# Kernel optimization log

Hardware: AMD Instinct MI355X
Metric: run time of the kernel (lower is better)

Reference implementation:

```python
import jax, jax.numpy as jnp
import numpy as np

B, S, D, E, N, K = 4, 2048, 1024, 2048, 16, 4

def setup_inputs() -> dict:
    key = jax.random.key(0)
    ks = jax.random.split(key, 16)
    w = lambda k, shape, s=0.02: jax.random.normal(k, shape, dtype=jnp.float32) * s
    return {
        "x": jax.random.normal(ks[0], (B, S, D), dtype=jnp.float32),
        "ln_g": jnp.ones((D,), jnp.float32),
        "ln_b": jnp.zeros((D,), jnp.float32),
        "W_in": w(ks[1], (2 * E, D)),
        "b_in": jnp.zeros((2 * E,), jnp.float32),
        "conv_w": w(ks[2], (E, 1, K), 0.1),
        "conv_b": jnp.zeros((E,), jnp.float32),
        "A": w(ks[3], (E, N), 0.1),
        "Bm": w(ks[4], (E, N), 0.1),
        "W_c": w(ks[5], (E, E)),
        "b_c": jnp.zeros((E,), jnp.float32),
        "W_d": w(ks[6], (E, E)),
        "b_d": jnp.zeros((E,), jnp.float32),
        "log_delta": jnp.zeros((E,), jnp.float32),
        "W_out": w(ks[7], (D, E)),
        "b_out": jnp.zeros((D,), jnp.float32),
    }

def _layernorm(x, g, b, eps=1e-5):
    mu = jnp.mean(x, axis=-1, keepdims=True)
    var = jnp.var(x, axis=-1, keepdims=True)
    return (x - mu) * jax.lax.rsqrt(var + eps) * g + b

def _forward(x, ln_g, ln_b, W_in, b_in, conv_w, conv_b, A, Bm, W_c, b_c, W_d, b_d, log_delta, W_out, b_out):
    x_ln = _layernorm(x, ln_g, ln_b)
    x_proj = jnp.einsum("bsd,ed->bse", x_ln, W_in) + b_in  # (B,S,2E)
    xp, gate = jnp.split(x_proj, 2, axis=-1)
    # causal depthwise conv1d (torch pads K-1 both sides then truncates -> left pad only)
    xc = jax.lax.conv_general_dilated(
        xp.transpose(0, 2, 1), conv_w, (1,), [(K - 1, 0)],
        dimension_numbers=("NCH", "OIH", "NCH"), feature_group_count=E)
    xc = (xc + conv_b[None, :, None]).transpose(0, 2, 1)  # (B,S,E)
    xc = jax.nn.silu(xc)
    # selective SSM
    delta = jax.nn.softplus(log_delta)
    A_diag = jnp.exp(-delta)  # (E,)
    u = (jnp.einsum("bse,fe->bsf", xc, W_c) + b_c) * jax.nn.sigmoid(jnp.einsum("bse,fe->bsf", xc, W_d) + b_d)
    def step(h, u_t):
        # h: (B,E,N), u_t: (B,E)
        h = h * A_diag[None, :, None] + u_t[:, :, None] * Bm[None]
        y = jnp.sum(h * A[None], axis=-1)  # (B,E)
        return h, y
    h0 = jnp.zeros((x.shape[0], E, N), x.dtype)
    _, ys = jax.lax.scan(step, h0, u.transpose(1, 0, 2))  # ys: (S,B,E)
    x_ssm = ys.transpose(1, 0, 2)
    x_gated = x_ssm * jax.nn.sigmoid(gate)
    out = jnp.einsum("bse,de->bsd", x_gated, W_out) + b_out
    return out + x

def reference(x, ln_g, ln_b, W_in, b_in, conv_w, conv_b, A, Bm, W_c, b_c, W_d, b_d, log_delta, W_out, b_out):
    return _forward(x, ln_g, ln_b, W_in, b_in, conv_w, conv_b, A, Bm, W_c, b_c, W_d, b_d, log_delta, W_out, b_out)
```

## Files before the change

### kernel.cpp

```cpp
#include <hip/hip_runtime.h>
#include <hip/hip_bf16.h>

typedef __bf16 bf16_t;
typedef unsigned char u8;
typedef float  f32x4  __attribute__((ext_vector_type(4)));
typedef int    i32x4  __attribute__((ext_vector_type(4)));
typedef int    i32x8  __attribute__((ext_vector_type(8)));
typedef __attribute__((address_space(3))) unsigned as3u32;
typedef __attribute__((address_space(1))) unsigned as1u32;

#define Bdim 4
#define Sdim 2048
#define Ddim 1024
#define Edim 2048
#define CH 64
#define CL 32

#define WSCALE 32.0f
#define XPSCALE 32.0f
#define XCSCALE 16.0f
#define CSCALE 16.0f
#define GSCALE 256.0f

__device__ __forceinline__ void gload_lds16(const void* g, void* l) {
  __builtin_amdgcn_global_load_lds((const as1u32*)g, (as3u32*)l, 16, 0, 0);
}
__device__ __forceinline__ float sigmoidf_(float x) {
  return 1.f / (1.f + __expf(-x));
}
__device__ __forceinline__ int pk_fp8x4(float a, float b, float c, float d) {
  int p = __builtin_amdgcn_cvt_pk_fp8_f32(a, b, 0, 0);
  p = __builtin_amdgcn_cvt_pk_fp8_f32(c, d, p, 1);
  return p;
}
template<int K>
__device__ __forceinline__ float dq8(int v) {
  return __builtin_amdgcn_cvt_f32_fp8(v, K);
}
__device__ __forceinline__ u8 q8(float v) {
  return (u8)(__builtin_amdgcn_cvt_pk_fp8_f32(v, v, 0, 0) & 0xff);
}

__global__ __launch_bounds__(256)
void cvt_fp8_3(const float* __restrict__ s0, const float* __restrict__ s1,
               const float* __restrict__ s2, u8* __restrict__ d0,
               u8* __restrict__ d1, u8* __restrict__ d2) {
  const int seg = blockIdx.x >> 12;
  const int i   = ((blockIdx.x & 4095) * 256 + threadIdx.x) * 4;
  const float* s = (seg == 0) ? s0 : (seg == 1) ? s1 : s2;
  u8*          d = (seg == 0) ? d0 : (seg == 1) ? d1 : d2;
  *(int*)(d + i) = pk_fp8x4(s[i] * WSCALE, s[i + 1] * WSCALE,
                            s[i + 2] * WSCALE, s[i + 3] * WSCALE);
}

__global__ __launch_bounds__(256)
void cvt_fp8(const float* __restrict__ s, u8* __restrict__ d, int n, float scale) {
  int i = (blockIdx.x * 256 + threadIdx.x) * 4;
  if (i < n)
    *(int*)(d + i) = pk_fp8x4(s[i] * scale, s[i + 1] * scale,
                              s[i + 2] * scale, s[i + 3] * scale);
}

__global__ __launch_bounds__(256)
void prep_scalars(const float* __restrict__ ld, const float* __restrict__ Am,
                  const float* __restrict__ Bm, float* __restrict__ aexp,
                  float* __restrict__ Ce) {
  int e = blockIdx.x * 256 + threadIdx.x;
  if (e >= Edim) return;
  float d = ld[e];
  float sp = (d > 20.f) ? d : log1pf(expf(d));
  aexp[e] = expf(-sp);
  float s = 0.f;
  #pragma unroll
  for (int n = 0; n < 16; ++n) s += Am[e * 16 + n] * Bm[e * 16 + n];
  Ce[e] = s;
}

__global__ __launch_bounds__(256)
void ln_kernel(const float* __restrict__ x, const float* __restrict__ g,
               const float* __restrict__ b, u8* __restrict__ out) {
  const int row = blockIdx.x;
  const int tid = threadIdx.x;
  const float4 v = ((const float4*)(x + (size_t)row * Ddim))[tid];
  float s  = v.x + v.y + v.z + v.w;
  float ss = v.x * v.x + v.y * v.y + v.z * v.z + v.w * v.w;
  #pragma unroll
  for (int o = 32; o > 0; o >>= 1) { s += __shfl_down(s, o); ss += __shfl_down(ss, o); }
  __shared__ float sh[8];
  const int wv = tid >> 6, lane = tid & 63;
  if (lane == 0) { sh[wv] = s; sh[4 + wv] = ss; }
  __syncthreads();
  s  = sh[0] + sh[1] + sh[2] + sh[3];
  ss = sh[4] + sh[5] + sh[6] + sh[7];
  const float mean = s * (1.f / Ddim);
  const float var  = ss * (1.f / Ddim) - mean * mean;
  const float rstd = rsqrtf(var + 1e-5f);
  const float4 gv = ((const float4*)g)[tid];
  const float4 bv = ((const float4*)b)[tid];
  *(int*)(out + (size_t)row * Ddim + tid * 4) =
      pk_fp8x4((v.x - mean) * rstd * gv.x + bv.x,
               (v.y - mean) * rstd * gv.y + bv.y,
               (v.z - mean) * rstd * gv.z + bv.z,
               (v.w - mean) * rstd * gv.w + bv.w);
}

#define BM 128
#define BN 128

template<int MODE>
__global__ __launch_bounds__(256)
void gemm_mx(const u8* __restrict__ A, const u8* __restrict__ Bw,
             const float* __restrict__ bias, const u8* __restrict__ X,
             const float* __restrict__ R, u8* __restrict__ C8,
             float* __restrict__ Cf, float descale, float oscale,
             int M, int N, int K) {
  __shared__ __align__(16) u8 As[BM * 256];
  __shared__ __align__(16) u8 Bs[BN * 256];

  const int tid  = threadIdx.x;
  const int lane = tid & 63;
  const int wv   = tid >> 6;
  const int m0   = blockIdx.y * BM;
  const int n0   = blockIdx.x * BN;

  const int wr = (wv >> 1) * 64;
  const int wc = (wv & 1) * 64;
  const int tq = lane >> 4;
  const int tr = lane & 15;

  f32x4 acc[4][4] = {};

  const int    srow  = tid >> 4;
  const int    sc16  = tid & 15;
  const int    shalf = sc16 >> 3;
  const int    s3    = (sc16 & 7) ^ (srow & 7);
  const size_t sBase = (size_t)srow * K + shalf * 128 + s3 * 16;
  const size_t rStep = (size_t)16 * K;
  const u8* Ap = A  + (size_t)m0 * K + sBase;
  const u8* Bp = Bw + (size_t)n0 * K + sBase;
  const int ldsW = wv * 1024;

  const int s7 = tr & 7;
  const int p0 = (((tq << 1)) ^ s7) * 16;
  const int p1 = (((tq << 1) | 1) ^ s7) * 16;

  for (int k0 = 0; k0 < K; k0 += 256) {
    __syncthreads();
    #pragma unroll
    for (int g = 0; g < 8; ++g)
      gload_lds16(Ap + g * rStep + k0, (u8*)As + g * 4096 + ldsW);
    #pragma unroll
    for (int g = 0; g < 8; ++g)
      gload_lds16(Bp + g * rStep + k0, (u8*)Bs + g * 4096 + ldsW);
    __syncthreads();

    #pragma unroll
    for (int kk = 0; kk < 256; kk += 128) {
      i32x8 aF[4], bF[4];
      #pragma unroll
      for (int i = 0; i < 4; ++i) {
        const int rb = (wr + i * 16 + tr) * 256 + kk;
        const i32x4 lo = *(const i32x4*)&As[rb + p0];
        const i32x4 hi = *(const i32x4*)&As[rb + p1];
        aF[i] = __builtin_shufflevector(lo, hi, 0, 1, 2, 3, 4, 5, 6, 7);
      }
      #pragma unroll
      for (int j = 0; j < 4; ++j) {
        const int rb = (wc + j * 16 + tr) * 256 + kk;
        const i32x4 lo = *(const i32x4*)&Bs[rb + p0];
        const i32x4 hi = *(const i32x4*)&Bs[rb + p1];
        bF[j] = __builtin_shufflevector(lo, hi, 0, 1, 2, 3, 4, 5, 6, 7);
      }
      #pragma unroll
      for (int i = 0; i < 4; ++i)
        #pragma unroll
        for (int j = 0; j < 4; ++j)
          acc[i][j] = __builtin_amdgcn_mfma_scale_f32_16x16x128_f8f6f4(
              aF[i], bF[j], acc[i][j], 0, 0, 0, 0x7F, 0, 0x7F);
    }
  }

  #pragma unroll
  for (int i = 0; i < 4; ++i) {
    #pragma unroll
    for (int j = 0; j < 4; ++j) {
      const int col = n0 + wc + j * 16 + tr;
      const float bv = bias[col];
      #pragma unroll
      for (int r = 0; r < 4; ++r) {
        const int rowg = m0 + wr + i * 16 + tq * 4 + r;
        const size_t idx = (size_t)rowg * N + col;
        const float v = acc[i][j][r] * descale + bv;
        if (MODE == 1) {
          Cf[idx] = v + R[idx];
        } else {
          C8[idx] = q8(v * oscale);
        }
      }
    }
  }
}

__global__ __launch_bounds__(256)
void gemm_cu(const u8* __restrict__ A, const u8* __restrict__ Wc8,
             const u8* __restrict__ Wd8, const float* __restrict__ bias_c,
             const float* __restrict__ bias_d, u8* __restrict__ U8,
             float descale, int M, int N, int K) {
  __shared__ __align__(16) u8 As[128 * 256];
  __shared__ __align__(16) u8 Bs[128 * 256];

  const int tid  = threadIdx.x;
  const int lane = tid & 63;
  const int wv   = tid >> 6;
  const int m0   = blockIdx.y * 128;
  const int n0   = blockIdx.x * 64;

  const int wr = (wv >> 1) * 64;
  const int wc = (wv & 1) * 32;
  const int tq = lane >> 4;
  const int tr = lane & 15;

  f32x4 accC[4][2] = {};
  f32x4 accD[4][2] = {};

  const int    srow  = tid >> 4;
  const int    sc16  = tid & 15;
  const int    shalf = sc16 >> 3;
  const int    s3    = (sc16 & 7) ^ (srow & 7);
  const size_t sBase = (size_t)srow * K + shalf * 128 + s3 * 16;
  const size_t rStep = (size_t)16 * K;
  const u8* Ap = A   + (size_t)m0 * K + sBase;
  const u8* Cp = Wc8 + (size_t)n0 * K + sBase;
  const u8* Dp = Wd8 + (size_t)n0 * K + sBase;
  const int ldsW = wv * 1024;

  const int s7 = tr & 7;
  const int p0 = (((tq << 1)) ^ s7) * 16;
  const int p1 = (((tq << 1) | 1) ^ s7) * 16;

  for (int k0 = 0; k0 < K; k0 += 256) {
    __syncthreads();
    #pragma unroll
    for (int g = 0; g < 8; ++g)
      gload_lds16(Ap + g * rStep + k0, (u8*)As + g * 4096 + ldsW);
    #pragma unroll
    for (int g = 0; g < 4; ++g)
      gload_lds16(Cp + g * rStep + k0, (u8*)Bs + g * 4096 + ldsW);
    #pragma unroll
    for (int g = 0; g < 4; ++g)
      gload_lds16(Dp + g * rStep + k0, (u8*)Bs + (4 + g) * 4096 + ldsW);
    __syncthreads();

    #pragma unroll
    for (int kk = 0; kk < 256; kk += 128) {
      i32x8 aF[4], bC[2], bD[2];
      #pragma unroll
      for (int j = 0; j < 2; ++j) {
        const int rbc = (wc + j * 16 + tr) * 256 + kk;
        const i32x4 loc = *(const i32x4*)&Bs[rbc + p0];
        const i32x4 hic = *(const i32x4*)&Bs[rbc + p1];
        bC[j] = __builtin_shufflevector(loc, hic, 0, 1, 2, 3, 4, 5, 6, 7);
        const int rbd = (64 + wc + j * 16 + tr) * 256 + kk;
        const i32x4 lod = *(const i32x4*)&Bs[rbd + p0];
        const i32x4 hid = *(const i32x4*)&Bs[rbd + p1];
        bD[j] = __builtin_shufflevector(lod, hid, 0, 1, 2, 3, 4, 5, 6, 7);
      }
      #pragma unroll
      for (int i = 0; i < 4; ++i) {
        const int rb = (wr + i * 16 + tr) * 256 + kk;
        const i32x4 lo = *(const i32x4*)&As[rb + p0];
        const i32x4 hi = *(const i32x4*)&As[rb + p1];
        aF[i] = __builtin_shufflevector(lo, hi, 0, 1, 2, 3, 4, 5, 6, 7);
      }
      #pragma unroll
      for (int i = 0; i < 4; ++i)
        #pragma unroll
        for (int j = 0; j < 2; ++j) {
          accC[i][j] = __builtin_amdgcn_mfma_scale_f32_16x16x128_f8f6f4(
              aF[i], bC[j], accC[i][j], 0, 0, 0, 0x7F, 0, 0x7F);
          accD[i][j] = __builtin_amdgcn_mfma_scale_f32_16x16x128_f8f6f4(
              aF[i], bD[j], accD[i][j], 0, 0, 0, 0x7F, 0, 0x7F);
        }
    }
  }

  #pragma unroll
  for (int i = 0; i < 4; ++i) {
    #pragma unroll
    for (int j = 0; j < 2; ++j) {
      const int col = n0 + wc + j * 16 + tr;
      const float bc = bias_c[col];
      const float bd = bias_d[col];
      #pragma unroll
      for (int r = 0; r < 4; ++r) {
        const int rowg = m0 + wr + i * 16 + tq * 4 + r;
        const size_t idx = (size_t)rowg * N + col;
        const float vc = accC[i][j][r] * descale + bc;
        const float vd = accD[i][j][r] * descale + bd;
        U8[idx] = q8(vc * CSCALE * sigmoidf_(vd));
      }
    }
  }
}

__global__ __launch_bounds__(256)
void conv_silu(const u8* __restrict__ xpg8, const float* __restrict__ cw,
               const float* __restrict__ cb, u8* __restrict__ xc8) {
  const int e0 = (blockIdx.y * 256 + threadIdx.x) * 4;
  const int b  = blockIdx.x >> 9;
  const int s0 = (blockIdx.x & 511) * 4;
  float w[4][4], bias[4];
  #pragma unroll
  for (int k = 0; k < 4; ++k) {
    const float4 wv = *(const float4*)(cw + (e0 + k) * 4);
    w[k][0] = wv.x; w[k][1] = wv.y; w[k][2] = wv.z; w[k][3] = wv.w;
    bias[k] = cb[e0 + k];
  }
  float f[7][4];
  #pragma unroll
  for (int j = 0; j < 7; ++j) {
    const int s = s0 - 3 + j;
    const int xv = (s >= 0) ? *(const int*)(xpg8 + (size_t)(b * Sdim + s) * (2 * Edim) + e0) : 0;
    f[j][0] = dq8<0>(xv); f[j][1] = dq8<1>(xv);
    f[j][2] = dq8<2>(xv); f[j][3] = dq8<3>(xv);
  }
  #pragma unroll
  for (int t = 0; t < 4; ++t) {
    float y[4];
    #pragma unroll
    for (int k = 0; k < 4; ++k) {
      float a = fmaf(w[k][0], f[t][k],
               fmaf(w[k][1], f[t + 1][k],
               fmaf(w[k][2], f[t + 2][k],
                    w[k][3] * f[t + 3][k])));
      a = a * (1.f / XPSCALE) + bias[k];
      y[k] = a * sigmoidf_(a) * XCSCALE;
    }
    *(int*)(xc8 + (size_t)(b * Sdim + s0 + t) * Edim + e0) =
        pk_fp8x4(y[0], y[1], y[2], y[3]);
  }
}

__global__ __launch_bounds__(256)
void scan_part1(const u8* __restrict__ u8p, const float* __restrict__ aexp,
                float* __restrict__ zloc) {
  const int c  = blockIdx.x;
  const int b  = blockIdx.y >> 1;
  const int e0 = ((blockIdx.y & 1) * 256 + threadIdx.x) * 4;
  const float4 av = *(const float4*)(aexp + e0);
  const u8* up = u8p + ((size_t)(b * Sdim + c * CL)) * Edim + e0;
  float z0 = 0.f, z1 = 0.f, z2 = 0.f, z3 = 0.f;
  #pragma unroll
  for (int t = 0; t < CL; ++t) {
    const int uv = *(const int*)(up + (size_t)t * Edim);
    z0 = fmaf(av.x, z0, dq8<0>(uv));
    z1 = fmaf(av.y, z1, dq8<1>(uv));
    z2 = fmaf(av.z, z2, dq8<2>(uv));
    z3 = fmaf(av.w, z3, dq8<3>(uv));
  }
  float4 zv = {z0, z1, z2, z3};
  *(float4*)(zloc + ((size_t)b * CH + c) * Edim + e0) = zv;
}

__global__ __launch_bounds__(256)
void scan_part2(const float* __restrict__ aexp, float* __restrict__ zloc) {
  const int idx = blockIdx.x * 256 + threadIdx.x;
  const int b = idx >> 11, e = idx & (Edim - 1);
  float a  = aexp[e];
  float aL = a * a;
  aL = aL * aL; aL = aL * aL; aL = aL * aL; aL = aL * aL;
  float* zp = zloc + (size_t)b * CH * Edim + e;
  float pref = 0.f;
  #pragma unroll 4
  for (int c = 0; c < CH; ++c) {
    const float loc = zp[(size_t)c * Edim];
    zp[(size_t)c * Edim] = pref;
    pref = fmaf(aL, pref, loc);
  }
}

__global__ __launch_bounds__(256)
void scan_part3(const u8* __restrict__ u8p, const u8* __restrict__ xpg8,
                const float* __restrict__ aexp, const float* __restrict__ Ce,
                const float* __restrict__ zloc, u8* __restrict__ xg8) {
  const int c  = blockIdx.x;
  const int b  = blockIdx.y >> 1;
  const int e0 = ((blockIdx.y & 1) * 256 + threadIdx.x) * 4;
  const float4 av = *(const float4*)(aexp + e0);
  float4 Cv = *(const float4*)(Ce + e0);
  const float cs = GSCALE / CSCALE;
  Cv.x *= cs; Cv.y *= cs; Cv.z *= cs; Cv.w *= cs;
  float4 zv = *(const float4*)(zloc + ((size_t)b * CH + c) * Edim + e0);
  const u8* up = u8p  + ((size_t)(b * Sdim + c * CL)) * Edim + e0;
  const u8* gp = xpg8 + ((size_t)(b * Sdim + c * CL)) * (2 * Edim) + Edim + e0;
  u8*       op = xg8  + ((size_t)(b * Sdim + c * CL)) * Edim + e0;
  #pragma unroll 4
  for (int t = 0; t < CL; ++t) {
    const int uv = *(const int*)(up + (size_t)t * Edim);
    const int gv = *(const int*)(gp + (size_t)t * (2 * Edim));
    zv.x = fmaf(av.x, zv.x, dq8<0>(uv));
    zv.y = fmaf(av.y, zv.y, dq8<1>(uv));
    zv.z = fmaf(av.z, zv.z, dq8<2>(uv));
    zv.w = fmaf(av.w, zv.w, dq8<3>(uv));
    const float y0 = Cv.x * zv.x * sigmoidf_(dq8<0>(gv) * (1.f / XPSCALE));
    const float y1 = Cv.y * zv.y * sigmoidf_(dq8<1>(gv) * (1.f / XPSCALE));
    const float y2 = Cv.z * zv.z * sigmoidf_(dq8<2>(gv) * (1.f / XPSCALE));
    const float y3 = Cv.w * zv.w * sigmoidf_(dq8<3>(gv) * (1.f / XPSCALE));
    *(int*)(op + (size_t)t * Edim) = pk_fp8x4(y0, y1, y2, y3);
  }
}

extern "C" void kernel_launch(void* const* d_in, const int* in_sizes, int n_in,
                              void* d_out, int out_size, void* d_ws, size_t ws_size,
                              hipStream_t stream) {
  const float* x         = (const float*)d_in[0];
  const float* ln_g      = (const float*)d_in[1];
  const float* ln_b      = (const float*)d_in[2];
  const float* W_in      = (const float*)d_in[3];
  const float* b_in      = (const float*)d_in[4];
  const float* conv_w    = (const float*)d_in[5];
  const float* conv_b    = (const float*)d_in[6];
  const float* Am        = (const float*)d_in[7];
  const float* Bm        = (const float*)d_in[8];
  const float* W_c       = (const float*)d_in[9];
  const float* b_c       = (const float*)d_in[10];
  const float* W_d       = (const float*)d_in[11];
  const float* b_d       = (const float*)d_in[12];
  const float* log_delta = (const float*)d_in[13];
  const float* W_out     = (const float*)d_in[14];
  const float* b_out     = (const float*)d_in[15];
  float* out = (float*)d_out;

  const size_t MiB = 1024 * 1024;
  char* w = (char*)d_ws;
  u8*     wWin8  = (u8*)   (w + 0);
  u8*     wWc8   = (u8*)   (w + 4 * MiB);
  u8*     wWd8   = (u8*)   (w + 8 * MiB);
  u8*     wWout8 = (u8*)   (w + 12 * MiB);
  float*  aexp   = (float*)(w + 15 * MiB);
  float*  Ce     = (float*)(w + 15 * MiB + 16384);
  float*  zloc   = (float*)(w + 15 * MiB + 65536);
  u8*     xln8   = (u8*)   (w + 18 * MiB);
  u8*     xpg8   = (u8*)   (w + 26 * MiB);
  u8*     xc8    = (u8*)   (w + 58 * MiB);
  u8*     u8b    = (u8*)   (w + 90 * MiB);
  u8*     xg8    = (u8*)   (w + 106 * MiB);

  const int M = Bdim * Sdim;
  const float dsIn  = 1.f / WSCALE;
  const float dsCD  = 1.f / (WSCALE * XCSCALE);
  const float dsOut = 1.f / (WSCALE * GSCALE);

  cvt_fp8_3<<<3 * 4096, 256, 0, stream>>>(W_in, W_c, W_d, wWin8, wWc8, wWd8);
  cvt_fp8<<<(Ddim * Edim) / 1024, 256, 0, stream>>>(W_out, wWout8, Ddim * Edim, WSCALE);
  prep_scalars<<<Edim / 256, 256, 0, stream>>>(log_delta, Am, Bm, aexp, Ce);

  ln_kernel<<<M, 256, 0, stream>>>(x, ln_g, ln_b, xln8);

  gemm_mx<3><<<dim3((2 * Edim) / BN, M / BM), 256, 0, stream>>>(
      xln8, wWin8, b_in, nullptr, nullptr, xpg8, nullptr, dsIn, XPSCALE, M, 2 * Edim, Ddim);

  conv_silu<<<dim3(Bdim * (Sdim / 4), Edim / 1024), 256, 0, stream>>>(xpg8, conv_w, conv_b, xc8);

  gemm_cu<<<dim3(Edim / 64, M / BM), 256, 0, stream>>>(
      xc8, wWc8, wWd8, b_c, b_d, u8b, dsCD, M, Edim, Edim);

  scan_part1<<<dim3(CH, Bdim * 2), 256, 0, stream>>>(u8b, aexp, zloc);
  scan_part2<<<(Bdim * Edim) / 256, 256, 0, stream>>>(aexp, zloc);
  scan_part3<<<dim3(CH, Bdim * 2), 256, 0, stream>>>(u8b, xpg8, aexp, Ce, zloc, xg8);

  gemm_mx<1><<<dim3(Ddim / BN, M / BM), 256, 0, stream>>>(
      xg8, wWout8, b_out, nullptr, x, nullptr, out, dsOut, 1.f, M, Ddim, Edim);

  (void)in_sizes; (void)n_in; (void)out_size; (void)ws_size;
}
```

Baseline: 353.1 us.

## Widen GEMM output tiles for in-projection and C/D projection kernels

```diff
diff --git a/kernel.cpp b/kernel.cpp
--- a/kernel.cpp
+++ b/kernel.cpp
@@ -202,33 +202,108 @@
 }
 
 __global__ __launch_bounds__(256)
+void gemm_mxw(const u8* __restrict__ A, const u8* __restrict__ Bw,
+              const float* __restrict__ bias, u8* __restrict__ C8,
+              float descale, float oscale, int M, int N, int K) {
+  __shared__ __align__(16) u8 As[128 * 128];
+  __shared__ __align__(16) u8 Bs[256 * 128];
+
+  const int tid  = threadIdx.x;
+  const int lane = tid & 63;
+  const int wv   = tid >> 6;
+  const int m0   = blockIdx.y * 128;
+  const int n0   = blockIdx.x * 256;
+  const int wr   = (wv >> 1) * 64;
+  const int wc   = (wv & 1) * 128;
+  const int tq   = lane >> 4;
+  const int tr   = lane & 15;
+
+  f32x4 acc[4][8] = {};
+
+  const int    srow = tid >> 3;
+  const int    scol = (tid & 7) ^ (srow & 7);
+  const size_t sBase = (size_t)srow * K + (size_t)scol * 16;
+  const size_t rStep = (size_t)32 * K;
+  const u8* Ap = A  + (size_t)m0 * K + sBase;
+  const u8* Bp = Bw + (size_t)n0 * K + sBase;
+  const int ldsW = wv * 1024;
+
+  const int s7 = tr & 7;
+  const int p0 = (((tq << 1)) ^ s7) * 16;
+  const int p1 = (((tq << 1) | 1) ^ s7) * 16;
+
+  for (int k0 = 0; k0 < K; k0 += 128) {
+    __syncthreads();
+    #pragma unroll
+    for (int g = 0; g < 4; ++g)
+      gload_lds16(Ap + g * rStep + k0, (u8*)As + g * 4096 + ldsW);
+    #pragma unroll
+    for (int g = 0; g < 8; ++g)
+      gload_lds16(Bp + g * rStep + k0, (u8*)Bs + g * 4096 + ldsW);
+    __syncthreads();
+
+    i32x8 aF[4];
+    #pragma unroll
+    for (int i = 0; i < 4; ++i) {
+      const int rb = (wr + i * 16 + tr) * 128;
+      const i32x4 lo = *(const i32x4*)&As[rb + p0];
+      const i32x4 hi = *(const i32x4*)&As[rb + p1];
+      aF[i] = __builtin_shufflevector(lo, hi, 0, 1, 2, 3, 4, 5, 6, 7);
+    }
+    #pragma unroll
+    for (int j = 0; j < 8; ++j) {
+      const int rb = (wc + j * 16 + tr) * 128;
+      const i32x4 lo = *(const i32x4*)&Bs[rb + p0];
+      const i32x4 hi = *(const i32x4*)&Bs[rb + p1];
+      const i32x8 bF = __builtin_shufflevector(lo, hi, 0, 1, 2, 3, 4, 5, 6, 7);
+      #pragma unroll
+      for (int i = 0; i < 4; ++i)
+        acc[i][j] = __builtin_amdgcn_mfma_scale_f32_16x16x128_f8f6f4(
+            aF[i], bF, acc[i][j], 0, 0, 0, 0x7F, 0, 0x7F);
+    }
+  }
+
+  #pragma unroll
+  for (int i = 0; i < 4; ++i) {
+    #pragma unroll
+    for (int j = 0; j < 8; ++j) {
+      const int col = n0 + wc + j * 16 + tr;
+      const float bv = bias[col];
+      #pragma unroll
+      for (int r = 0; r < 4; ++r) {
+        const int rowg = m0 + wr + i * 16 + tq * 4 + r;
+        const size_t idx = (size_t)rowg * N + col;
+        C8[idx] = q8((acc[i][j][r] * descale + bv) * oscale);
+      }
+    }
+  }
+}
+
+__global__ __launch_bounds__(256)
 void gemm_cu(const u8* __restrict__ A, const u8* __restrict__ Wc8,
              const u8* __restrict__ Wd8, const float* __restrict__ bias_c,
              const float* __restrict__ bias_d, u8* __restrict__ U8,
              float descale, int M, int N, int K) {
-  __shared__ __align__(16) u8 As[128 * 256];
-  __shared__ __align__(16) u8 Bs[128 * 256];
+  __shared__ __align__(16) u8 As[128 * 128];
+  __shared__ __align__(16) u8 Bs[256 * 128];
 
   const int tid  = threadIdx.x;
   const int lane = tid & 63;
   const int wv   = tid >> 6;
   const int m0   = blockIdx.y * 128;
-  const int n0   = blockIdx.x * 64;
-
-  const int wr = (wv >> 1) * 64;
-  const int wc = (wv & 1) * 32;
-  const int tq = lane >> 4;
-  const int tr = lane & 15;
-
-  f32x4 accC[4][2] = {};
-  f32x4 accD[4][2] = {};
-
-  const int    srow  = tid >> 4;
-  const int    sc16  = tid & 15;
-  const int    shalf = sc16 >> 3;
-  const int    s3    = (sc16 & 7) ^ (srow & 7);
-  const size_t sBase = (size_t)srow * K + shalf * 128 + s3 * 16;
-  const size_t rStep = (size_t)16 * K;
+  const int n0   = blockIdx.x * 128;
+  const int wr   = (wv >> 1) * 64;
+  const int wc   = (wv & 1) * 64;
+  const int tq   = lane >> 4;
+  const int tr   = lane & 15;
+
+  f32x4 accC[4][4] = {};
+  f32x4 accD[4][4] = {};
+
+  const int    srow = tid >> 3;
+  const int    scol = (tid & 7) ^ (srow & 7);
+  const size_t sBase = (size_t)srow * K + (size_t)scol * 16;
+  const size_t rStep = (size_t)32 * K;
   const u8* Ap = A   + (size_t)m0 * K + sBase;
   const u8* Cp = Wc8 + (size_t)n0 * K + sBase;
   const u8* Dp = Wd8 + (size_t)n0 * K + sBase;
@@ -238,10 +313,10 @@
   const int p0 = (((tq << 1)) ^ s7) * 16;
   const int p1 = (((tq << 1) | 1) ^ s7) * 16;
 
-  for (int k0 = 0; k0 < K; k0 += 256) {
+  for (int k0 = 0; k0 < K; k0 += 128) {
     __syncthreads();
     #pragma unroll
-    for (int g = 0; g < 8; ++g)
+    for (int g = 0; g < 4; ++g)
       gload_lds16(Ap + g * rStep + k0, (u8*)As + g * 4096 + ldsW);
     #pragma unroll
     for (int g = 0; g < 4; ++g)
@@ -251,43 +326,39 @@
       gload_lds16(Dp + g * rStep + k0, (u8*)Bs + (4 + g) * 4096 + ldsW);
     __syncthreads();
 
-    #pragma unroll
-    for (int kk = 0; kk < 256; kk += 128) {
-      i32x8 aF[4], bC[2], bD[2];
-      #pragma unroll
-      for (int j = 0; j < 2; ++j) {
-        const int rbc = (wc + j * 16 + tr) * 256 + kk;
-        const i32x4 loc = *(const i32x4*)&Bs[rbc + p0];
-        const i32x4 hic = *(const i32x4*)&Bs[rbc + p1];
-        bC[j] = __builtin_shufflevector(loc, hic, 0, 1, 2, 3, 4, 5, 6, 7);
-        const int rbd = (64 + wc + j * 16 + tr) * 256 + kk;
-        const i32x4 lod = *(const i32x4*)&Bs[rbd + p0];
-        const i32x4 hid = *(const i32x4*)&Bs[rbd + p1];
-        bD[j] = __builtin_shufflevector(lod, hid, 0, 1, 2, 3, 4, 5, 6, 7);
-      }
-      #pragma unroll
-      for (int i = 0; i < 4; ++i) {
-        const int rb = (wr + i * 16 + tr) * 256 + kk;
-        const i32x4 lo = *(const i32x4*)&As[rb + p0];
-        const i32x4 hi = *(const i32x4*)&As[rb + p1];
-        aF[i] = __builtin_shufflevector(lo, hi, 0, 1, 2, 3, 4, 5, 6, 7);
-      }
+    i32x8 aF[4];
+    #pragma unroll
+    for (int i = 0; i < 4; ++i) {
+      const int rb = (wr + i * 16 + tr) * 128;
+      const i32x4 lo = *(const i32x4*)&As[rb + p0];
+      const i32x4 hi = *(const i32x4*)&As[rb + p1];
+      aF[i] = __builtin_shufflevector(lo, hi, 0, 1, 2, 3, 4, 5, 6, 7);
+    }
+    #pragma unroll
+    for (int j = 0; j < 4; ++j) {
+      const int rbc = (wc + j * 16 + tr) * 128;
+      const i32x4 loc = *(const i32x4*)&Bs[rbc + p0];
+      const i32x4 hic = *(const i32x4*)&Bs[rbc + p1];
+      const i32x8 bC = __builtin_shufflevector(loc, hic, 0, 1, 2, 3, 4, 5, 6, 7);
       #pragma unroll
       for (int i = 0; i < 4; ++i)
-        #pragma unroll
-        for (int j = 0; j < 2; ++j) {
-          accC[i][j] = __builtin_amdgcn_mfma_scale_f32_16x16x128_f8f6f4(
-              aF[i], bC[j], accC[i][j], 0, 0, 0, 0x7F, 0, 0x7F);
-          accD[i][j] = __builtin_amdgcn_mfma_scale_f32_16x16x128_f8f6f4(
-              aF[i], bD[j], accD[i][j], 0, 0, 0, 0x7F, 0, 0x7F);
-        }
+        accC[i][j] = __builtin_amdgcn_mfma_scale_f32_16x16x128_f8f6f4(
+            aF[i], bC, accC[i][j], 0, 0, 0, 0x7F, 0, 0x7F);
+      const int rbd = ((128 + wc + j * 16 + tr)) * 128;
+      const i32x4 lod = *(const i32x4*)&Bs[rbd + p0];
+      const i32x4 hid = *(const i32x4*)&Bs[rbd + p1];
+      const i32x8 bD = __builtin_shufflevector(lod, hid, 0, 1, 2, 3, 4, 5, 6, 7);
+      #pragma unroll
+      for (int i = 0; i < 4; ++i)
+        accD[i][j] = __builtin_amdgcn_mfma_scale_f32_16x16x128_f8f6f4(
+            aF[i], bD, accD[i][j], 0, 0, 0, 0x7F, 0, 0x7F);
     }
   }
 
   #pragma unroll
   for (int i = 0; i < 4; ++i) {
     #pragma unroll
-    for (int j = 0; j < 2; ++j) {
+    for (int j = 0; j < 4; ++j) {
       const int col = n0 + wc + j * 16 + tr;
       const float bc = bias_c[col];
       const float bd = bias_d[col];
@@ -457,12 +528,12 @@
 
   ln_kernel<<<M, 256, 0, stream>>>(x, ln_g, ln_b, xln8);
 
-  gemm_mx<3><<<dim3((2 * Edim) / BN, M / BM), 256, 0, stream>>>(
-      xln8, wWin8, b_in, nullptr, nullptr, xpg8, nullptr, dsIn, XPSCALE, M, 2 * Edim, Ddim);
+  gemm_mxw<<<dim3((2 * Edim) / 256, M / 128), 256, 0, stream>>>(
+      xln8, wWin8, b_in, xpg8, dsIn, XPSCALE, M, 2 * Edim, Ddim);
 
   conv_silu<<<dim3(Bdim * (Sdim / 4), Edim / 1024), 256, 0, stream>>>(xpg8, conv_w, conv_b, xc8);
 
-  gemm_cu<<<dim3(Edim / 64, M / BM), 256, 0, stream>>>(
+  gemm_cu<<<dim3(Edim / 128, M / 128), 256, 0, stream>>>(
       xc8, wWc8, wWd8, b_c, b_d, u8b, dsCD, M, Edim, Edim);
 
   scan_part1<<<dim3(CH, Bdim * 2), 256, 0, stream>>>(u8b, aexp, zloc);
```

New measurement: 416.2 us. 1.18x slower.

## Double-buffer LDS in gemm_cu with async prefetch two K-tiles ahead

Applied to the files above, without the earlier changes.

```diff
diff --git a/kernel.cpp b/kernel.cpp
--- a/kernel.cpp
+++ b/kernel.cpp
@@ -201,13 +201,59 @@
   }
 }
 
+#define CUTILE(AS, BS, t_)                                                     \
+  {                                                                            \
+    i32x8 aF[4], bC[2], bD[2];                                                 \
+    _Pragma("unroll") for (int j_ = 0; j_ < 2; ++j_) {                         \
+      const int rbc = (wc + j_ * 16 + tr) * 128;                               \
+      const i32x4 loc = *(const i32x4*)&(BS)[rbc + p0];                        \
+      const i32x4 hic = *(const i32x4*)&(BS)[rbc + p1];                        \
+      bC[j_] = __builtin_shufflevector(loc, hic, 0, 1, 2, 3, 4, 5, 6, 7);      \
+      const int rbd = (64 + wc + j_ * 16 + tr) * 128;                          \
+      const i32x4 lod = *(const i32x4*)&(BS)[rbd + p0];                        \
+      const i32x4 hid = *(const i32x4*)&(BS)[rbd + p1];                        \
+      bD[j_] = __builtin_shufflevector(lod, hid, 0, 1, 2, 3, 4, 5, 6, 7);      \
+    }                                                                          \
+    _Pragma("unroll") for (int i_ = 0; i_ < 4; ++i_) {                         \
+      const int rb = (wr + i_ * 16 + tr) * 128;                                \
+      const i32x4 lo = *(const i32x4*)&(AS)[rb + p0];                          \
+      const i32x4 hi = *(const i32x4*)&(AS)[rb + p1];                          \
+      aF[i_] = __builtin_shufflevector(lo, hi, 0, 1, 2, 3, 4, 5, 6, 7);        \
+    }                                                                          \
+    __builtin_amdgcn_s_setprio(1);                                             \
+    _Pragma("unroll") for (int i_ = 0; i_ < 4; ++i_)                           \
+      _Pragma("unroll") for (int j_ = 0; j_ < 2; ++j_) {                       \
+        accC[i_][j_] = __builtin_amdgcn_mfma_scale_f32_16x16x128_f8f6f4(       \
+            aF[i_], bC[j_], accC[i_][j_], 0, 0, 0, 0x7F, 0, 0x7F);             \
+        accD[i_][j_] = __builtin_amdgcn_mfma_scale_f32_16x16x128_f8f6f4(       \
+            aF[i_], bD[j_], accD[i_][j_], 0, 0, 0, 0x7F, 0, 0x7F);             \
+      }                                                                        \
+    __builtin_amdgcn_s_setprio(0);                                             \
+    __builtin_amdgcn_s_barrier();                                              \
+    if ((t_) + 2 < NK) {                                                       \
+      const size_t ko_ = (size_t)((t_) + 2) * 128;                             \
+      _Pragma("unroll") for (int g_ = 0; g_ < 4; ++g_)                         \
+        gload_lds16(Ap + g_ * rStep + ko_, (u8*)(AS) + g_ * 4096 + ldsW);      \
+      gload_lds16(Cp + ko_,         (u8*)(BS) + 0 * 4096 + ldsW);              \
+      gload_lds16(Cp + rStep + ko_, (u8*)(BS) + 1 * 4096 + ldsW);              \
+      gload_lds16(Dp + ko_,         (u8*)(BS) + 2 * 4096 + ldsW);              \
+      gload_lds16(Dp + rStep + ko_, (u8*)(BS) + 3 * 4096 + ldsW);              \
+      asm volatile("s_waitcnt vmcnt(8)" ::: "memory");                         \
+    } else {                                                                   \
+      asm volatile("s_waitcnt vmcnt(0)" ::: "memory");                         \
+    }                                                                          \
+    __builtin_amdgcn_s_barrier();                                              \
+  }
+
 __global__ __launch_bounds__(256)
 void gemm_cu(const u8* __restrict__ A, const u8* __restrict__ Wc8,
              const u8* __restrict__ Wd8, const float* __restrict__ bias_c,
              const float* __restrict__ bias_d, u8* __restrict__ U8,
              float descale, int M, int N, int K) {
-  __shared__ __align__(16) u8 As[128 * 256];
-  __shared__ __align__(16) u8 Bs[128 * 256];
+  __shared__ __align__(16) u8 As0[128 * 128];
+  __shared__ __align__(16) u8 Bs0[128 * 128];
+  __shared__ __align__(16) u8 As1[128 * 128];
+  __shared__ __align__(16) u8 Bs1[128 * 128];
 
   const int tid  = threadIdx.x;
   const int lane = tid & 63;
@@ -223,12 +269,10 @@
   f32x4 accC[4][2] = {};
   f32x4 accD[4][2] = {};
 
-  const int    srow  = tid >> 4;
-  const int    sc16  = tid & 15;
-  const int    shalf = sc16 >> 3;
-  const int    s3    = (sc16 & 7) ^ (srow & 7);
-  const size_t sBase = (size_t)srow * K + shalf * 128 + s3 * 16;
-  const size_t rStep = (size_t)16 * K;
+  const int    srow = tid >> 3;
+  const int    scol = (tid & 7) ^ (srow & 7);
+  const size_t sBase = (size_t)srow * K + (size_t)scol * 16;
+  const size_t rStep = (size_t)32 * K;
   const u8* Ap = A   + (size_t)m0 * K + sBase;
   const u8* Cp = Wc8 + (size_t)n0 * K + sBase;
   const u8* Dp = Wd8 + (size_t)n0 * K + sBase;
@@ -238,50 +282,29 @@
   const int p0 = (((tq << 1)) ^ s7) * 16;
   const int p1 = (((tq << 1) | 1) ^ s7) * 16;
 
-  for (int k0 = 0; k0 < K; k0 += 256) {
-    __syncthreads();
-    #pragma unroll
-    for (int g = 0; g < 8; ++g)
-      gload_lds16(Ap + g * rStep + k0, (u8*)As + g * 4096 + ldsW);
-    #pragma unroll
-    for (int g = 0; g < 4; ++g)
-      gload_lds16(Cp + g * rStep + k0, (u8*)Bs + g * 4096 + ldsW);
-    #pragma unroll
-    for (int g = 0; g < 4; ++g)
-      gload_lds16(Dp + g * rStep + k0, (u8*)Bs + (4 + g) * 4096 + ldsW);
-    __syncthreads();
-
-    #pragma unroll
-    for (int kk = 0; kk < 256; kk += 128) {
-      i32x8 aF[4], bC[2], bD[2];
-      #pragma unroll
-      for (int j = 0; j < 2; ++j) {
-        const int rbc = (wc + j * 16 + tr) * 256 + kk;
-        const i32x4 loc = *(const i32x4*)&Bs[rbc + p0];
-        const i32x4 hic = *(const i32x4*)&Bs[rbc + p1];
-        bC[j] = __builtin_shufflevector(loc, hic, 0, 1, 2, 3, 4, 5, 6, 7);
-        const int rbd = (64 + wc + j * 16 + tr) * 256 + kk;
-        const i32x4 lod = *(const i32x4*)&Bs[rbd + p0];
-        const i32x4 hid = *(const i32x4*)&Bs[rbd + p1];
-        bD[j] = __builtin_shufflevector(lod, hid, 0, 1, 2, 3, 4, 5, 6, 7);
-      }
-      #pragma unroll
-      for (int i = 0; i < 4; ++i) {
-        const int rb = (wr + i * 16 + tr) * 256 + kk;
-        const i32x4 lo = *(const i32x4*)&As[rb + p0];
-        const i32x4 hi = *(const i32x4*)&As[rb + p1];
-        aF[i] = __builtin_shufflevector(lo, hi, 0, 1, 2, 3, 4, 5, 6, 7);
-      }
-      #pragma unroll
-      for (int i = 0; i < 4; ++i)
-        #pragma unroll
-        for (int j = 0; j < 2; ++j) {
-          accC[i][j] = __builtin_amdgcn_mfma_scale_f32_16x16x128_f8f6f4(
-              aF[i], bC[j], accC[i][j], 0, 0, 0, 0x7F, 0, 0x7F);
-          accD[i][j] = __builtin_amdgcn_mfma_scale_f32_16x16x128_f8f6f4(
-              aF[i], bD[j], accD[i][j], 0, 0, 0, 0x7F, 0, 0x7F);
-        }
-    }
+  const int NK = K >> 7;
+
+  #pragma unroll
+  for (int g = 0; g < 4; ++g)
+    gload_lds16(Ap + g * rStep, (u8*)As0 + g * 4096 + ldsW);
+  gload_lds16(Cp,         (u8*)Bs0 + 0 * 4096 + ldsW);
+  gload_lds16(Cp + rStep, (u8*)Bs0 + 1 * 4096 + ldsW);
+  gload_lds16(Dp,         (u8*)Bs0 + 2 * 4096 + ldsW);
+  gload_lds16(Dp + rStep, (u8*)Bs0 + 3 * 4096 + ldsW);
+  #pragma unroll
+  for (int g = 0; g < 4; ++g)
+    gload_lds16(Ap + g * rStep + 128, (u8*)As1 + g * 4096 + ldsW);
+  gload_lds16(Cp + 128,         (u8*)Bs1 + 0 * 4096 + ldsW);
+  gload_lds16(Cp + rStep + 128, (u8*)Bs1 + 1 * 4096 + ldsW);
+  gload_lds16(Dp + 128,         (u8*)Bs1 + 2 * 4096 + ldsW);
+  gload_lds16(Dp + rStep + 128, (u8*)Bs1 + 3 * 4096 + ldsW);
+  asm volatile("s_waitcnt vmcnt(8)" ::: "memory");
+  __builtin_amdgcn_s_barrier();
+
+  for (int tp = 0; tp < (NK >> 1); ++tp) {
+    const int t0 = tp * 2;
+    CUTILE(As0, Bs0, t0);
+    CUTILE(As1, Bs1, t0 + 1);
   }
 
   #pragma unroll
```

Result: no change. 351.2 us (-0.5%).
